# Kernel tuning notes

Hardware: AMD Instinct MI355X
Metric: run time of the kernel (lower is better)

Reference implementation:

```python
import jax, jax.numpy as jnp
import numpy as np

N, E, F_IN, H, D = 50000, 800000, 128, 4, 32
NEG_SLOPE = 0.2

def setup_inputs() -> dict:
    key = jax.random.key(0)
    ks = jax.random.split(key, 8)
    x = jax.random.normal(ks[0], (N, F_IN), dtype=jnp.float32)
    src = jax.random.randint(ks[1], (E,), 0, N, dtype=jnp.int32)
    dst = jax.random.randint(ks[2], (E,), 0, N, dtype=jnp.int32)
    s = 1.0 / np.sqrt(F_IN)
    W_src = jax.random.uniform(ks[3], (F_IN, H * D), jnp.float32, -s, s)
    b_src = jnp.zeros((H * D,), jnp.float32)
    W_dst = jax.random.uniform(ks[4], (F_IN, H * D), jnp.float32, -s, s)
    b_dst = jnp.zeros((H * D,), jnp.float32)
    attn = jax.random.normal(ks[5], (H, D), dtype=jnp.float32) / np.sqrt(D)
    return {"x": x, "src": src, "dst": dst, "W_src": W_src, "b_src": b_src,
            "W_dst": W_dst, "b_dst": b_dst, "attn": attn}

def reference(x, src, dst, W_src, b_src, W_dst, b_dst, attn):
    n = x.shape[0]
    # dense projections: [N, H, D]
    fs = (x @ W_src + b_src).reshape(n, H, D)
    fd = (x @ W_dst + b_dst).reshape(n, H, D)
    # GATv2 edge score: a^T leaky_relu(W_l x_u + W_r x_v)
    e = jax.nn.leaky_relu(fs[src] + fd[dst], NEG_SLOPE)  # [E, H, D]
    score = jnp.einsum('ehd,hd->eh', e, attn)            # [E, H]
    # segment softmax over incoming edges of each dst node
    smax = jax.ops.segment_max(score, dst, num_segments=n)
    smax = jnp.where(jnp.isfinite(smax), smax, 0.0)
    ex = jnp.exp(score - smax[dst])
    denom = jax.ops.segment_sum(ex, dst, num_segments=n)
    alpha = ex / denom[dst]                              # [E, H]
    # scatter-weighted aggregation of src features
    h = jax.ops.segment_sum(alpha[:, :, None] * fs[src], dst, num_segments=n)
    h = jax.nn.relu(h)                                   # activation=relu
    return h.reshape(n, H * D)
```

## Files before the change

kernel.cpp:

```cpp
#include <hip/hip_runtime.h>
#include <hip/hip_fp16.h>

#define NN 50000
#define NE 800000
#define FIN 128
#define NH 4
#define HD 32
#define FOUT 128
#define NEG 0.2f
#define NB_EDGE ((NE + 255) / 256)
#define NB_W    ((256 * FIN + 255) / 256)
#define N_GEMM  (391 * 4)
#define NBKT    98
#define CHUNK   4096
#define NCHUNK  ((NE + CHUNK - 1) / CHUNK)
#define BCAP    12288

typedef __attribute__((ext_vector_type(8))) short bf16x8;
typedef __attribute__((ext_vector_type(4))) float f32x4;

__device__ __forceinline__ ushort f2bf(float f) {
    uint u = __float_as_uint(f);
    u += 0x7FFF + ((u >> 16) & 1);
    return (ushort)(u >> 16);
}

template<int CTRL>
__device__ __forceinline__ float dpp_add(float x) {
    int y = __builtin_amdgcn_update_dpp(0, __float_as_int(x), CTRL, 0xF, 0xF, false);
    return x + __int_as_float(y);
}
#define DPP_QUAD_XOR1 0xB1
#define DPP_QUAD_XOR2 0x4E

__device__ __forceinline__ __half2 u2h(uint u) { return __builtin_bit_cast(__half2, u); }
__device__ __forceinline__ uint h2u(__half2 h) { return __builtin_bit_cast(uint, h); }

__device__ __forceinline__ __half2 hmax2(__half2 a, __half2 b) {
    uint r, ua = h2u(a), ub = h2u(b);
    asm("v_pk_max_f16 %0, %1, %2" : "=v"(r) : "v"(ua), "v"(ub));
    return u2h(r);
}

__global__ __launch_bounds__(256) void conv_all_k(
    const float* __restrict__ x, ushort* __restrict__ xb,
    const float* __restrict__ Wsrc, const float* __restrict__ Wdst,
    ushort* __restrict__ Wt)
{
    const int b = blockIdx.x;
    if (b < NB_EDGE) {
        int i = b * 256 + threadIdx.x;
        if (i >= NE) return;
        float4 a = ((const float4*)x)[2 * i];
        float4 c = ((const float4*)x)[2 * i + 1];
        uint4 o;
        o.x = (uint)f2bf(a.x) | ((uint)f2bf(a.y) << 16);
        o.y = (uint)f2bf(a.z) | ((uint)f2bf(a.w) << 16);
        o.z = (uint)f2bf(c.x) | ((uint)f2bf(c.y) << 16);
        o.w = (uint)f2bf(c.z) | ((uint)f2bf(c.w) << 16);
        *(uint4*)&xb[8 * i] = o;
    } else {
        int t = (b - NB_EDGE) * 256 + threadIdx.x;
        if (t >= 256 * FIN) return;
        int n = t >> 7, k = t & 127;
        float v = (n < 128) ? Wsrc[k * 128 + n] : Wdst[k * 128 + (n - 128)];
        Wt[t] = f2bf(v);
    }
}

__global__ __launch_bounds__(256) void gemm_hist_k(
    const ushort* __restrict__ xb, const ushort* __restrict__ Wt,
    const float* __restrict__ bsrc, const float* __restrict__ bdst,
    __half* __restrict__ fsfd,
    const int* __restrict__ dst, int* __restrict__ chunk_hist)
{
    __shared__ ushort As[128 * 128];
    __shared__ ushort Bs[64 * 128];
    __shared__ int hist[NBKT];
    const int b = blockIdx.x;
    const int tid = threadIdx.x;

    if (b < NCHUNK) {
        const int e0 = b * CHUNK;
        for (int t = tid; t < NBKT; t += 256) hist[t] = 0;
        __syncthreads();
        #pragma unroll
        for (int k = 0; k < 16; ++k) {
            const int e = e0 + k * 256 + tid;
            if (e < NE) atomicAdd(&hist[dst[e] >> 9], 1);
        }
        __syncthreads();
        for (int t = tid; t < NBKT; t += 256)
            chunk_hist[b * NBKT + t] = hist[t];
        return;
    }

    const int g = b - NCHUNK;
    const int bm = (g >> 2) * 128;
    const int bn = (g & 3) * 64;

    for (int q = tid; q < 128 * 16; q += 256) {
        int r = q >> 4, c16 = q & 15;
        int row = bm + r;
        uint4 v = make_uint4(0u, 0u, 0u, 0u);
        if (row < NN) v = *(const uint4*)&xb[row * FIN + c16 * 8];
        int off = r * 256 + ((c16 * 16) ^ ((r & 7) << 4));
        *(uint4*)((char*)As + off) = v;
    }
    for (int q = tid; q < 64 * 16; q += 256) {
        int r = q >> 4, c16 = q & 15;
        uint4 v = *(const uint4*)&Wt[(bn + r) * FIN + c16 * 8];
        int off = r * 256 + ((c16 * 16) ^ ((r & 7) << 4));
        *(uint4*)((char*)Bs + off) = v;
    }
    __syncthreads();

    const int wid = tid >> 6, lane = tid & 63;
    const int wr = (wid >> 1) * 64, wc = (wid & 1) * 32;
    const int lrow = lane & 15;
    const int lk = (lane >> 4) * 16;

    f32x4 acc[4][2] = {};
    #pragma unroll
    for (int kk = 0; kk < 4; ++kk) {
        bf16x8 a[4], bb[2];
        #pragma unroll
        for (int m = 0; m < 4; ++m) {
            int r = wr + m * 16 + lrow;
            int off = r * 256 + ((kk * 64 + lk) ^ ((r & 7) << 4));
            a[m] = *(bf16x8*)((char*)As + off);
        }
        #pragma unroll
        for (int n = 0; n < 2; ++n) {
            int r = wc + n * 16 + lrow;
            int off = r * 256 + ((kk * 64 + lk) ^ ((r & 7) << 4));
            bb[n] = *(bf16x8*)((char*)Bs + off);
        }
        #pragma unroll
        for (int m = 0; m < 4; ++m)
            #pragma unroll
            for (int n = 0; n < 2; ++n)
                acc[m][n] = __builtin_amdgcn_mfma_f32_16x16x32_bf16(a[m], bb[n], acc[m][n], 0, 0, 0);
    }

    #pragma unroll
    for (int m = 0; m < 4; ++m) {
        #pragma unroll
        for (int n = 0; n < 2; ++n) {
            int gcol = bn + wc + n * 16 + (lane & 15);
            float bias = (gcol < 128) ? bsrc[gcol] : bdst[gcol - 128];
            #pragma unroll
            for (int r = 0; r < 4; ++r) {
                int grow = bm + wr + m * 16 + (lane >> 4) * 4 + r;
                if (grow < NN)
                    fsfd[(size_t)grow * 256 + gcol] = __float2half(acc[m][n][r] + bias);
            }
        }
    }
}

__global__ __launch_bounds__(256) void scan_chunks_k(
    const int* __restrict__ chunk_hist, int* __restrict__ chunk_base, int* __restrict__ btotal)
{
    __shared__ int sh[256];
    const int b = blockIdx.x, t = threadIdx.x;
    const int v = (t < NCHUNK) ? chunk_hist[t * NBKT + b] : 0;
    sh[t] = v;
    __syncthreads();
    for (int off = 1; off < 256; off <<= 1) {
        int add = (t >= off) ? sh[t - off] : 0;
        __syncthreads();
        sh[t] += add;
        __syncthreads();
    }
    if (t < NCHUNK) chunk_base[t * NBKT + b] = sh[t] - v;
    if (t == 255) btotal[b] = sh[255];
}

__global__ __launch_bounds__(256) void scan_buckets_k(
    const int* __restrict__ btotal, int* __restrict__ bkbase,
    const float* __restrict__ attn, __half* __restrict__ attn_h)
{
    __shared__ int sh[256];
    const int t = threadIdx.x;
    const int v = (t < NBKT) ? btotal[t] : 0;
    sh[t] = v;
    __syncthreads();
    for (int off = 1; off < 256; off <<= 1) {
        int add = (t >= off) ? sh[t - off] : 0;
        __syncthreads();
        sh[t] += add;
        __syncthreads();
    }
    if (t < NBKT) bkbase[t] = sh[t] - v;
    if (t == 0) bkbase[NBKT] = NE;
    if (t < FOUT) attn_h[t] = __float2half(attn[t]);
}

__global__ __launch_bounds__(256) void scatter_k(
    const int* __restrict__ dst, const int* __restrict__ src,
    const int* __restrict__ bkbase, const int* __restrict__ chunk_base,
    uint* __restrict__ ebuf)
{
    __shared__ int cur[NBKT];
    const int chunk = blockIdx.x;
    const int tid = threadIdx.x;
    for (int t = tid; t < NBKT; t += 256)
        cur[t] = bkbase[t] + chunk_base[chunk * NBKT + t];
    __syncthreads();
    const int e0 = chunk * CHUNK;
    #pragma unroll
    for (int k = 0; k < 16; ++k) {
        const int e = e0 + k * 256 + tid;
        if (e < NE) {
            const int d = dst[e];
            const int p = atomicAdd(&cur[d >> 9], 1);
            ebuf[p] = ((uint)d << 16) | (uint)src[e];
        }
    }
}

__global__ __launch_bounds__(256) void binB_k(
    const uint* __restrict__ ebuf, const int* __restrict__ bkbase,
    int* __restrict__ rowptr, ushort* __restrict__ nbr)
{
    __shared__ int cnt_s[512];
    __shared__ int ps[256];
    __shared__ ushort buf[BCAP];
    const int b = blockIdx.x;
    const int tid = threadIdx.x;
    const int node0 = b << 9;
    const int nodes = (node0 + 512 < NN) ? 512 : (NN - node0);
    const int segbase = bkbase[b];
    const int segend  = bkbase[b + 1];
    const int seglen  = segend - segbase;

    cnt_s[tid] = 0;
    cnt_s[tid + 256] = 0;
    __syncthreads();
    for (int i = segbase + tid; i < segend; i += 256)
        atomicAdd(&cnt_s[(int)(ebuf[i] >> 16) - node0], 1);
    __syncthreads();

    const int c0 = cnt_s[2 * tid], c1 = cnt_s[2 * tid + 1];
    const int pair = c0 + c1;
    ps[tid] = pair;
    __syncthreads();
    for (int off = 1; off < 256; off <<= 1) {
        int add = (tid >= off) ? ps[tid - off] : 0;
        __syncthreads();
        ps[tid] += add;
        __syncthreads();
    }
    const int ex = ps[tid] - pair;
    __syncthreads();
    cnt_s[2 * tid] = ex;
    cnt_s[2 * tid + 1] = ex + c0;
    if (2 * tid < nodes)     rowptr[node0 + 2 * tid]     = segbase + ex;
    if (2 * tid + 1 < nodes) rowptr[node0 + 2 * tid + 1] = segbase + ex + c0;
    if (b == NBKT - 1 && tid == 0) rowptr[NN] = segend;
    __syncthreads();

    if (seglen <= BCAP) {
        for (int i = segbase + tid; i < segend; i += 256) {
            const uint e = ebuf[i];
            const int d = (int)(e >> 16) - node0;
            const int p = atomicAdd(&cnt_s[d], 1);
            buf[p] = (ushort)(e & 0xffffu);
        }
        __syncthreads();
        for (int i = tid; i < seglen; i += 256)
            nbr[segbase + i] = buf[i];
    } else {
        for (int i = segbase + tid; i < segend; i += 256) {
            const uint e = ebuf[i];
            const int d = (int)(e >> 16) - node0;
            const int p = atomicAdd(&cnt_s[d], 1);
            nbr[segbase + p] = (ushort)(e & 0xffffu);
        }
    }
}

__global__ __launch_bounds__(256) void gat_node_k(
    const __half* __restrict__ fsfd, const __half* __restrict__ attn_h,
    const int* __restrict__ rowptr, const ushort* __restrict__ nbr,
    float* __restrict__ out)
{
    const int node = blockIdx.x * 4 + (threadIdx.x >> 6);
    const int lane = threadIdx.x & 63;
    const int ql = lane & 15;
    const int q  = lane >> 4;

    const uint4 ufd = *(const uint4*)&fsfd[(size_t)node * 256 + 128 + 8 * ql];
    const __half2 fd0 = u2h(ufd.x), fd1 = u2h(ufd.y), fd2 = u2h(ufd.z), fd3 = u2h(ufd.w);
    const uint4 uav = *(const uint4*)&attn_h[8 * ql];
    const __half2 av0 = u2h(uav.x), av1 = u2h(uav.y), av2 = u2h(uav.z), av3 = u2h(uav.w);
    const __half2 k02 = __float2half2_rn(NEG);

    const int beg = rowptr[node];
    const int end = rowptr[node + 1];

    float den = 0.f;
    __half2 acc0 = u2h(0), acc1 = u2h(0), acc2 = u2h(0), acc3 = u2h(0);

    for (int i = beg; i < end; i += 8) {
        #pragma unroll
        for (int j = 0; j < 2; ++j) {
            const int idx = i + 4 * j + q;
            const bool valid = idx < end;
            const int s = nbr[valid ? idx : end - 1];
            const uint4 u = *(const uint4*)&fsfd[(size_t)s * 256 + 8 * ql];
            const __half2 f0 = u2h(u.x), f1 = u2h(u.y), f2 = u2h(u.z), f3 = u2h(u.w);
            __half2 v0 = __hadd2(f0, fd0), v1 = __hadd2(f1, fd1);
            __half2 v2 = __hadd2(f2, fd2), v3 = __hadd2(f3, fd3);
            v0 = hmax2(v0, __hmul2(v0, k02));
            v1 = hmax2(v1, __hmul2(v1, k02));
            v2 = hmax2(v2, __hmul2(v2, k02));
            v3 = hmax2(v3, __hmul2(v3, k02));
            __half2 sch = __hmul2(v0, av0);
            sch = __hfma2(v1, av1, sch);
            sch = __hfma2(v2, av2, sch);
            sch = __hfma2(v3, av3, sch);
            float sc = __low2float(sch) + __high2float(sch);
            sc = dpp_add<DPP_QUAD_XOR1>(sc);
            sc = dpp_add<DPP_QUAD_XOR2>(sc);
            float ex = __expf(sc);
            ex = valid ? ex : 0.f;
            den += ex;
            const __half2 exh = __float2half2_rn(ex);
            acc0 = __hfma2(exh, f0, acc0);
            acc1 = __hfma2(exh, f1, acc1);
            acc2 = __hfma2(exh, f2, acc2);
            acc3 = __hfma2(exh, f3, acc3);
        }
    }

    den += __shfl_xor(den, 16, 64);
    den += __shfl_xor(den, 32, 64);
    uint ua0 = h2u(acc0), ua1 = h2u(acc1), ua2 = h2u(acc2), ua3 = h2u(acc3);
    ua0 = h2u(__hadd2(u2h(ua0), u2h((uint)__shfl_xor((int)ua0, 16, 64))));
    ua1 = h2u(__hadd2(u2h(ua1), u2h((uint)__shfl_xor((int)ua1, 16, 64))));
    ua2 = h2u(__hadd2(u2h(ua2), u2h((uint)__shfl_xor((int)ua2, 16, 64))));
    ua3 = h2u(__hadd2(u2h(ua3), u2h((uint)__shfl_xor((int)ua3, 16, 64))));
    ua0 = h2u(__hadd2(u2h(ua0), u2h((uint)__shfl_xor((int)ua0, 32, 64))));
    ua1 = h2u(__hadd2(u2h(ua1), u2h((uint)__shfl_xor((int)ua1, 32, 64))));
    ua2 = h2u(__hadd2(u2h(ua2), u2h((uint)__shfl_xor((int)ua2, 32, 64))));
    ua3 = h2u(__hadd2(u2h(ua3), u2h((uint)__shfl_xor((int)ua3, 32, 64))));

    if (q == 0) {
        const float inv = (den > 0.f) ? 1.f / den : 0.f;
        float4 o0, o1;
        o0.x = fmaxf(__low2float(u2h(ua0))  * inv, 0.f);
        o0.y = fmaxf(__high2float(u2h(ua0)) * inv, 0.f);
        o0.z = fmaxf(__low2float(u2h(ua1))  * inv, 0.f);
        o0.w = fmaxf(__high2float(u2h(ua1)) * inv, 0.f);
        o1.x = fmaxf(__low2float(u2h(ua2))  * inv, 0.f);
        o1.y = fmaxf(__high2float(u2h(ua2)) * inv, 0.f);
        o1.z = fmaxf(__low2float(u2h(ua3))  * inv, 0.f);
        o1.w = fmaxf(__high2float(u2h(ua3)) * inv, 0.f);
        *(float4*)&out[(size_t)node * FOUT + 8 * ql] = o0;
        *(float4*)&out[(size_t)node * FOUT + 8 * ql + 4] = o1;
    }
}

extern "C" void kernel_launch(void* const* d_in, const int* in_sizes, int n_in,
                              void* d_out, int out_size, void* d_ws, size_t ws_size,
                              hipStream_t stream)
{
    const float* x    = (const float*)d_in[0];
    const int*   src  = (const int*)d_in[1];
    const int*   dst  = (const int*)d_in[2];
    const float* Wsrc = (const float*)d_in[3];
    const float* bsrc = (const float*)d_in[4];
    const float* Wdst = (const float*)d_in[5];
    const float* bdst = (const float*)d_in[6];
    const float* attn = (const float*)d_in[7];
    float* out = (float*)d_out;

    ushort* xb      = (ushort*)d_ws;
    ushort* Wt      = xb + (size_t)NN * FIN;
    __half* fsfd    = (__half*)(Wt + 256 * FIN);
    int* chunk_hist = (int*)(fsfd + (size_t)NN * 256);
    int* chunk_base = chunk_hist + NCHUNK * NBKT;
    int* btotal     = chunk_base + NCHUNK * NBKT;
    int* bkbase     = btotal + NBKT;
    int* rowptr     = bkbase + NBKT + 1;
    uint* ebuf      = (uint*)(rowptr + NN + 1);
    ushort* nbr     = (ushort*)(ebuf + NE);
    __half* attn_h  = (__half*)(nbr + NE);

    conv_all_k<<<NB_EDGE + NB_W, 256, 0, stream>>>(x, xb, Wsrc, Wdst, Wt);
    gemm_hist_k<<<NCHUNK + N_GEMM, 256, 0, stream>>>(xb, Wt, bsrc, bdst, fsfd,
                                                     dst, chunk_hist);
    scan_chunks_k<<<NBKT, 256, 0, stream>>>(chunk_hist, chunk_base, btotal);
    scan_buckets_k<<<1, 256, 0, stream>>>(btotal, bkbase, attn, attn_h);
    scatter_k<<<NCHUNK, 256, 0, stream>>>(dst, src, bkbase, chunk_base, ebuf);
    binB_k<<<NBKT, 256, 0, stream>>>(ebuf, bkbase, rowptr, nbr);
    gat_node_k<<<(NN + 3) / 4, 256, 0, stream>>>(fsfd, attn_h, rowptr, nbr, out);
}
```

Baseline: 102.7 us.

## Fuse x bf16 conversion into GEMM and co-schedule GEMM with edge scatter

```diff
diff --git a/kernel.cpp b/kernel.cpp
--- a/kernel.cpp
+++ b/kernel.cpp
@@ -8,22 +8,23 @@
 #define HD 32
 #define FOUT 128
 #define NEG 0.2f
-#define NB_EDGE ((NE + 255) / 256)
 #define NB_W    ((256 * FIN + 255) / 256)
 #define N_GEMM  (391 * 4)
 #define NBKT    98
 #define CHUNK   4096
 #define NCHUNK  ((NE + CHUNK - 1) / CHUNK)
+#define GB_GRID (NCHUNK * 9)
 #define BCAP    12288
 
 typedef __attribute__((ext_vector_type(8))) short bf16x8;
 typedef __attribute__((ext_vector_type(4))) float f32x4;
 
-__device__ __forceinline__ ushort f2bf(float f) {
+__device__ __forceinline__ uint f2bf_u(float f) {
     uint u = __float_as_uint(f);
     u += 0x7FFF + ((u >> 16) & 1);
-    return (ushort)(u >> 16);
-}
+    return u >> 16;
+}
+__device__ __forceinline__ ushort f2bf(float f) { return (ushort)f2bf_u(f); }
 
 template<int CTRL>
 __device__ __forceinline__ float dpp_add(float x) {
@@ -42,25 +43,28 @@
     return u2h(r);
 }
 
-__global__ __launch_bounds__(256) void conv_all_k(
-    const float* __restrict__ x, ushort* __restrict__ xb,
+__global__ __launch_bounds__(256) void hist_wt_k(
+    const int* __restrict__ dst, int* __restrict__ chunk_hist,
     const float* __restrict__ Wsrc, const float* __restrict__ Wdst,
     ushort* __restrict__ Wt)
 {
+    __shared__ int hist[NBKT];
     const int b = blockIdx.x;
-    if (b < NB_EDGE) {
-        int i = b * 256 + threadIdx.x;
-        if (i >= NE) return;
-        float4 a = ((const float4*)x)[2 * i];
-        float4 c = ((const float4*)x)[2 * i + 1];
-        uint4 o;
-        o.x = (uint)f2bf(a.x) | ((uint)f2bf(a.y) << 16);
-        o.y = (uint)f2bf(a.z) | ((uint)f2bf(a.w) << 16);
-        o.z = (uint)f2bf(c.x) | ((uint)f2bf(c.y) << 16);
-        o.w = (uint)f2bf(c.z) | ((uint)f2bf(c.w) << 16);
-        *(uint4*)&xb[8 * i] = o;
+    const int tid = threadIdx.x;
+    if (b < NCHUNK) {
+        const int e0 = b * CHUNK;
+        for (int t = tid; t < NBKT; t += 256) hist[t] = 0;
+        __syncthreads();
+        #pragma unroll
+        for (int k = 0; k < 16; ++k) {
+            const int e = e0 + k * 256 + tid;
+            if (e < NE) atomicAdd(&hist[dst[e] >> 9], 1);
+        }
+        __syncthreads();
+        for (int t = tid; t < NBKT; t += 256)
+            chunk_hist[b * NBKT + t] = hist[t];
     } else {
-        int t = (b - NB_EDGE) * 256 + threadIdx.x;
+        int t = (b - NCHUNK) * 256 + tid;
         if (t >= 256 * FIN) return;
         int n = t >> 7, k = t & 127;
         float v = (n < 128) ? Wsrc[k * 128 + n] : Wdst[k * 128 + (n - 128)];
@@ -68,44 +72,95 @@
     }
 }
 
-__global__ __launch_bounds__(256) void gemm_hist_k(
-    const ushort* __restrict__ xb, const ushort* __restrict__ Wt,
+__global__ __launch_bounds__(256) void scan_chunks_k(
+    const int* __restrict__ chunk_hist, int* __restrict__ chunk_base, int* __restrict__ btotal)
+{
+    __shared__ int sh[256];
+    const int b = blockIdx.x, t = threadIdx.x;
+    const int v = (t < NCHUNK) ? chunk_hist[t * NBKT + b] : 0;
+    sh[t] = v;
+    __syncthreads();
+    for (int off = 1; off < 256; off <<= 1) {
+        int add = (t >= off) ? sh[t - off] : 0;
+        __syncthreads();
+        sh[t] += add;
+        __syncthreads();
+    }
+    if (t < NCHUNK) chunk_base[t * NBKT + b] = sh[t] - v;
+    if (t == 255) btotal[b] = sh[255];
+}
+
+__global__ __launch_bounds__(256) void scan_buckets_k(
+    const int* __restrict__ btotal, int* __restrict__ bkbase,
+    const float* __restrict__ attn, __half* __restrict__ attn_h)
+{
+    __shared__ int sh[256];
+    const int t = threadIdx.x;
+    const int v = (t < NBKT) ? btotal[t] : 0;
+    sh[t] = v;
+    __syncthreads();
+    for (int off = 1; off < 256; off <<= 1) {
+        int add = (t >= off) ? sh[t - off] : 0;
+        __syncthreads();
+        sh[t] += add;
+        __syncthreads();
+    }
+    if (t < NBKT) bkbase[t] = sh[t] - v;
+    if (t == 0) bkbase[NBKT] = NE;
+    if (t < FOUT) attn_h[t] = __float2half(attn[t]);
+}
+
+__global__ __launch_bounds__(256) void gemm_scatter_k(
+    const float* __restrict__ x, const ushort* __restrict__ Wt,
     const float* __restrict__ bsrc, const float* __restrict__ bdst,
     __half* __restrict__ fsfd,
-    const int* __restrict__ dst, int* __restrict__ chunk_hist)
+    const int* __restrict__ dst, const int* __restrict__ src,
+    const int* __restrict__ bkbase, const int* __restrict__ chunk_base,
+    uint* __restrict__ ebuf)
 {
     __shared__ ushort As[128 * 128];
     __shared__ ushort Bs[64 * 128];
-    __shared__ int hist[NBKT];
+    __shared__ int cur[NBKT];
     const int b = blockIdx.x;
     const int tid = threadIdx.x;
 
-    if (b < NCHUNK) {
-        const int e0 = b * CHUNK;
-        for (int t = tid; t < NBKT; t += 256) hist[t] = 0;
-        __syncthreads();
+    if (b % 9 == 0) {
+        const int chunk = b / 9;
+        for (int t = tid; t < NBKT; t += 256)
+            cur[t] = bkbase[t] + chunk_base[chunk * NBKT + t];
+        __syncthreads();
+        const int e0 = chunk * CHUNK;
         #pragma unroll
         for (int k = 0; k < 16; ++k) {
             const int e = e0 + k * 256 + tid;
-            if (e < NE) atomicAdd(&hist[dst[e] >> 9], 1);
-        }
-        __syncthreads();
-        for (int t = tid; t < NBKT; t += 256)
-            chunk_hist[b * NBKT + t] = hist[t];
+            if (e < NE) {
+                const int d = dst[e];
+                const int p = atomicAdd(&cur[d >> 9], 1);
+                ebuf[p] = ((uint)d << 16) | (uint)src[e];
+            }
+        }
         return;
     }
 
-    const int g = b - NCHUNK;
+    const int g = b - b / 9 - 1;
+    if (g >= N_GEMM) return;
     const int bm = (g >> 2) * 128;
     const int bn = (g & 3) * 64;
 
     for (int q = tid; q < 128 * 16; q += 256) {
         int r = q >> 4, c16 = q & 15;
         int row = bm + r;
-        uint4 v = make_uint4(0u, 0u, 0u, 0u);
-        if (row < NN) v = *(const uint4*)&xb[row * FIN + c16 * 8];
+        uint4 o = make_uint4(0u, 0u, 0u, 0u);
+        if (row < NN) {
+            const float4 a = *(const float4*)&x[(size_t)row * FIN + c16 * 8];
+            const float4 c = *(const float4*)&x[(size_t)row * FIN + c16 * 8 + 4];
+            o.x = f2bf_u(a.x) | (f2bf_u(a.y) << 16);
+            o.y = f2bf_u(a.z) | (f2bf_u(a.w) << 16);
+            o.z = f2bf_u(c.x) | (f2bf_u(c.y) << 16);
+            o.w = f2bf_u(c.z) | (f2bf_u(c.w) << 16);
+        }
         int off = r * 256 + ((c16 * 16) ^ ((r & 7) << 4));
-        *(uint4*)((char*)As + off) = v;
+        *(uint4*)((char*)As + off) = o;
     }
     for (int q = tid; q < 64 * 16; q += 256) {
         int r = q >> 4, c16 = q & 15;
@@ -155,67 +210,6 @@
                 if (grow < NN)
                     fsfd[(size_t)grow * 256 + gcol] = __float2half(acc[m][n][r] + bias);
             }
-        }
-    }
-}
-
-__global__ __launch_bounds__(256) void scan_chunks_k(
-    const int* __restrict__ chunk_hist, int* __restrict__ chunk_base, int* __restrict__ btotal)
-{
-    __shared__ int sh[256];
-    const int b = blockIdx.x, t = threadIdx.x;
-    const int v = (t < NCHUNK) ? chunk_hist[t * NBKT + b] : 0;
-    sh[t] = v;
-    __syncthreads();
-    for (int off = 1; off < 256; off <<= 1) {
-        int add = (t >= off) ? sh[t - off] : 0;
-        __syncthreads();
-        sh[t] += add;
-        __syncthreads();
-    }
-    if (t < NCHUNK) chunk_base[t * NBKT + b] = sh[t] - v;
-    if (t == 255) btotal[b] = sh[255];
-}
-
-__global__ __launch_bounds__(256) void scan_buckets_k(
-    const int* __restrict__ btotal, int* __restrict__ bkbase,
-    const float* __restrict__ attn, __half* __restrict__ attn_h)
-{
-    __shared__ int sh[256];
-    const int t = threadIdx.x;
-    const int v = (t < NBKT) ? btotal[t] : 0;
-    sh[t] = v;
-    __syncthreads();
-    for (int off = 1; off < 256; off <<= 1) {
-        int add = (t >= off) ? sh[t - off] : 0;
-        __syncthreads();
-        sh[t] += add;
-        __syncthreads();
-    }
-    if (t < NBKT) bkbase[t] = sh[t] - v;
-    if (t == 0) bkbase[NBKT] = NE;
-    if (t < FOUT) attn_h[t] = __float2half(attn[t]);
-}
-
-__global__ __launch_bounds__(256) void scatter_k(
-    const int* __restrict__ dst, const int* __restrict__ src,
-    const int* __restrict__ bkbase, const int* __restrict__ chunk_base,
-    uint* __restrict__ ebuf)
-{
-    __shared__ int cur[NBKT];
-    const int chunk = blockIdx.x;
-    const int tid = threadIdx.x;
-    for (int t = tid; t < NBKT; t += 256)
-        cur[t] = bkbase[t] + chunk_base[chunk * NBKT + t];
-    __syncthreads();
-    const int e0 = chunk * CHUNK;
-    #pragma unroll
-    for (int k = 0; k < 16; ++k) {
-        const int e = e0 + k * 256 + tid;
-        if (e < NE) {
-            const int d = dst[e];
-            const int p = atomicAdd(&cur[d >> 9], 1);
-            ebuf[p] = ((uint)d << 16) | (uint)src[e];
         }
     }
 }
@@ -303,9 +297,9 @@
     float den = 0.f;
     __half2 acc0 = u2h(0), acc1 = u2h(0), acc2 = u2h(0), acc3 = u2h(0);
 
-    for (int i = beg; i < end; i += 8) {
-        #pragma unroll
-        for (int j = 0; j < 2; ++j) {
+    for (int i = beg; i < end; i += 16) {
+        #pragma unroll
+        for (int j = 0; j < 4; ++j) {
             const int idx = i + 4 * j + q;
             const bool valid = idx < end;
             const int s = nbr[valid ? idx : end - 1];
@@ -377,8 +371,7 @@
     const float* attn = (const float*)d_in[7];
     float* out = (float*)d_out;
 
-    ushort* xb      = (ushort*)d_ws;
-    ushort* Wt      = xb + (size_t)NN * FIN;
+    ushort* Wt      = (ushort*)d_ws;
     __half* fsfd    = (__half*)(Wt + 256 * FIN);
     int* chunk_hist = (int*)(fsfd + (size_t)NN * 256);
     int* chunk_base = chunk_hist + NCHUNK * NBKT;
@@ -389,12 +382,11 @@
     ushort* nbr     = (ushort*)(ebuf + NE);
     __half* attn_h  = (__half*)(nbr + NE);
 
-    conv_all_k<<<NB_EDGE + NB_W, 256, 0, stream>>>(x, xb, Wsrc, Wdst, Wt);
-    gemm_hist_k<<<NCHUNK + N_GEMM, 256, 0, stream>>>(xb, Wt, bsrc, bdst, fsfd,
-                                                     dst, chunk_hist);
+    hist_wt_k<<<NCHUNK + NB_W, 256, 0, stream>>>(dst, chunk_hist, Wsrc, Wdst, Wt);
     scan_chunks_k<<<NBKT, 256, 0, stream>>>(chunk_hist, chunk_base, btotal);
     scan_buckets_k<<<1, 256, 0, stream>>>(btotal, bkbase, attn, attn_h);
-    scatter_k<<<NCHUNK, 256, 0, stream>>>(dst, src, bkbase, chunk_base, ebuf);
+    gemm_scatter_k<<<GB_GRID, 256, 0, stream>>>(x, Wt, bsrc, bdst, fsfd,
+                                                dst, src, bkbase, chunk_base, ebuf);
     binB_k<<<NBKT, 256, 0, stream>>>(ebuf, bkbase, rowptr, nbr);
     gat_node_k<<<(NN + 3) / 4, 256, 0, stream>>>(fsfd, attn_h, rowptr, nbr, out);
 }
```

Result: faster. 98.48 us (-4.2%).
